# Optimization experiments

Measured on AMD Instinct MI355X. Metric: run time of the kernel, lower is better.

Reference implementation:

```python
import jax, jax.numpy as jnp
import numpy as np

B, N, L, K = 2, 16384, 256, 4
DIN, DOUT, DLAT, H, A, NH = 2, 3, 64, 128, 32, 4
PI = float(np.pi)

def _lin(key, din, dout, std=None):
    k1, k2 = jax.random.split(key)
    if std is None:
        lim = 1.0 / np.sqrt(din)
        w = jax.random.uniform(k1, (din, dout), minval=-lim, maxval=lim)
        b = jax.random.uniform(k2, (dout,), minval=-lim, maxval=lim)
        return w, b
    return jax.random.normal(k1, (din, dout)) * std

def setup_inputs() -> dict:
    key = jax.random.key(0)
    ks = jax.random.split(key, 16)
    x = jax.random.uniform(ks[0], (B, N, DIN)) * 2.0 - 1.0
    p = jax.random.uniform(ks[1], (B, L, DIN)) * 2.0 - 1.0
    c = jax.random.normal(ks[2], (B, L, DLAT))
    g = jax.random.uniform(ks[3], (B, L, 1)) * 0.5 + 0.1
    W_stem, b_stem = _lin(ks[4], DLAT, H)
    Wq_sin = _lin(ks[5], DIN, H // 2, std=2.0)
    Wq1, bq1 = _lin(ks[6], H + DIN, H)
    Wq2, bq2 = _lin(ks[7], H, NH * A)
    Wv_sin = _lin(ks[8], DIN, H // 2, std=20.0)
    Wv1, bv1 = _lin(ks[9], H + DIN, H)
    Wv2, bv2 = _lin(ks[10], H, 2 * H)
    Wk, bk = _lin(ks[11], H, NH * A)
    Wv, bv = _lin(ks[12], H, NH * H)
    Wo1, bo1 = _lin(ks[13], NH * H, NH * H)
    Wo2, bo2 = _lin(ks[14], NH * H, DOUT)
    return dict(x=x, p=p, c=c, g=g, W_stem=W_stem, b_stem=b_stem,
                Wq_sin=Wq_sin, Wq1=Wq1, bq1=bq1, Wq2=Wq2, bq2=bq2,
                Wv_sin=Wv_sin, Wv1=Wv1, bv1=bv1, Wv2=Wv2, bv2=bv2,
                Wk=Wk, bk=bk, Wv=Wv, bv=bv, Wo1=Wo1, bo1=bo1, Wo2=Wo2, bo2=bo2)

def _sin_emb(coords, W):
    c = PI * (coords + 1.0)
    e = c @ W
    return jnp.sin(jnp.concatenate([c, e, e + PI / 2.0], axis=-1))

def _emb_mlp(coords, Wsin, W1, b1, W2, b2):
    h = _sin_emb(coords, Wsin)
    h = jax.nn.gelu(h @ W1 + b1, approximate=False)
    return h @ W2 + b2

def _gather(t, idx):
    # t: [B,L,D], idx: [B,N,K] -> [B,N,K,D]
    return jax.vmap(lambda tb, ib: tb[ib])(t, idx)

def reference(x, p, c, g, W_stem, b_stem, Wq_sin, Wq1, bq1, Wq2, bq2,
              Wv_sin, Wv1, bv1, Wv2, bv2, Wk, bk, Wv, bv, Wo1, bo1, Wo2, bo2):
    c = c @ W_stem + b_stem                       # [B,L,H]
    k = c @ Wk + bk                               # [B,L,NH*A]
    rel_pos = x[:, :, None, :] - p[:, None, :, :] # [B,N,L,2]
    zx = jnp.sum(rel_pos ** 2, axis=-1)           # [B,N,L]
    idx = jnp.argsort(zx, axis=-1)[:, :, :K]      # [B,N,K]
    zx_k = jnp.take_along_axis(zx, idx, axis=2)[..., None]            # [B,N,K,1]
    rel_k = jnp.take_along_axis(rel_pos, idx[..., None], axis=2)      # [B,N,K,2]
    c_k = _gather(c, idx)                         # [B,N,K,H]
    k_k = _gather(k, idx)                         # [B,N,K,NH*A]
    g_k = _gather(g, idx)                         # [B,N,K,1]
    q = _emb_mlp(rel_k, Wq_sin, Wq1, bq1, Wq2, bq2)                   # [B,N,K,NH*A]
    vgb = _emb_mlp(rel_k, Wv_sin, Wv1, bv1, Wv2, bv2)                 # [B,N,K,2H]
    v_g, v_b = vgb[..., :H], vgb[..., H:]
    v = (c_k * v_g + v_b) @ Wv + bv               # [B,N,K,NH*H]
    q = q.reshape(B, N, K, NH, A)
    k_k = k_k.reshape(B, N, K, NH, A)
    v = v.reshape(B, N, K, NH, H)
    logits = jnp.sum(q * k_k, axis=-1, keepdims=True) \
             - ((1.0 / g_k ** 2) * zx_k)[..., None, :]                # [B,N,K,NH,1]
    att = jax.nn.softmax(logits, axis=2)
    y = jnp.sum(att * v, axis=2).reshape(B, N, NH * H)
    y = jax.nn.gelu(y @ Wo1 + bo1, approximate=False)
    return y @ Wo2 + bo2                          # [B,N,3]
```

## Files before the change

kernel.cpp:

```cpp
#include <hip/hip_runtime.h>
#include <math.h>

typedef unsigned short U16;
typedef unsigned int u32;
typedef unsigned long long u64;
typedef __attribute__((ext_vector_type(8))) short short8;
typedef __attribute__((ext_vector_type(4))) float f4;

#define LPTS   256
#define MFMA16(a,b,c) __builtin_amdgcn_mfma_f32_16x16x32_bf16(a, b, c, 0, 0, 0)

__device__ __forceinline__ float bf2f(U16 u) {
  return __uint_as_float(((unsigned int)u) << 16);
}
__device__ __forceinline__ U16 f2bf(float f) {
  unsigned int x = __float_as_uint(f);
  return (U16)((x + 0x7fffu + ((x >> 16) & 1u)) >> 16);
}
__device__ __forceinline__ float gelu_f(float v) {
  float z = fabsf(v) * 0.70710678f;
  float t = __builtin_amdgcn_rcpf(fmaf(0.3275911f, z, 1.0f));
  float poly = t * fmaf(t, fmaf(t, fmaf(t, fmaf(t, 1.061405429f, -1.453152027f),
                                        1.421413741f), -0.284496736f), 0.254829592f);
  float e = __expf(-z * z);
  float erf_abs = fmaf(-poly, e, 1.0f);
  float erf_s = copysignf(erf_abs, v);
  return 0.5f * v * (1.0f + erf_s);
}
__device__ __forceinline__ void ins4(u32& k0, u32& k1, u32& k2, u32& k3, u32 key) {
  if (key < k3) {
    if (key < k0)      { k3 = k2; k2 = k1; k1 = k0; k0 = key; }
    else if (key < k1) { k3 = k2; k2 = k1; k1 = key; }
    else if (key < k2) { k3 = k2; k2 = key; }
    else               { k3 = key; }
  }
}
__device__ __forceinline__ float ldf(const void* s, int i, int mode) {
  return mode ? bf2f(((const U16*)s)[i]) : ((const float*)s)[i];
}
__device__ __forceinline__ int wave_sniff(const void* w4) {
  int lane = threadIdx.x & 63;
  float v = bf2f(((const U16*)w4)[2 * lane]);
  u64 m = __ballot(fabsf(v) <= 0.1251f);
  return (__popcll(m) >= 56) ? 1 : 0;
}

struct PackArgs {
  const void* src[6];
  int K[6], N[6], KS[6];
  int base[7];
};

__global__ __launch_bounds__(256) void enf_prep(PackArgs pa,
    const void* c, const void* Wst, const void* bst, const void* Wkp, const void* bkp,
    float* __restrict__ cp_ws, float* __restrict__ kk_ws, U16* __restrict__ P)
{
  __shared__ float c_s[2][64];
  __shared__ float cp_s[2][128];
  const int t = threadIdx.x;
  const int mode = wave_sniff(Wst);
  const int bid = blockIdx.x;
  if (bid < 204) {
    int u = bid * 256 + t;
    if (u < pa.base[6]) {
      int s = 0;
      while (u >= pa.base[s + 1]) ++s;
      int rel = u - pa.base[s];
      int lane8 = rel & 63, rest = rel >> 6;
      int ks = rest % pa.KS[s], nt = rest / pa.KS[s];
      int kb = ks * 32 + ((lane8 >> 4) * 8);
      int n  = nt * 16 + (lane8 & 15);
      U16 vv[8];
#pragma unroll
      for (int j = 0; j < 8; ++j) {
        int k = kb + j;
        U16 v = 0;
        if (k < pa.K[s]) {
          int off = k * pa.N[s] + n;
          v = mode ? ((const U16*)pa.src[s])[off] : f2bf(((const float*)pa.src[s])[off]);
        }
        vv[j] = v;
      }
      *(short8*)(P + (size_t)u * 8) = *(short8*)vv;
    }
  } else {
    const int half = t >> 7, tl = t & 127;
    const int row = (bid - 204) * 2 + half;
    if (tl < 64) c_s[half][tl] = ldf(c, row * 64 + tl, mode);
    __syncthreads();
    float acc = 0.f;
#pragma unroll 8
    for (int i = 0; i < 64; ++i) acc = fmaf(c_s[half][i], ldf(Wst, i * 128 + tl, mode), acc);
    float cpv = acc + ldf(bst, tl, mode);
    cp_s[half][tl] = cpv;
    cp_ws[row * 128 + tl] = cpv;
    __syncthreads();
    acc = 0.f;
#pragma unroll 8
    for (int i = 0; i < 128; ++i) acc = fmaf(cp_s[half][i], ldf(Wkp, i * 128 + tl, mode), acc);
    kk_ws[row * 128 + tl] = acc + ldf(bkp, tl, mode);
  }
}

__global__ __launch_bounds__(512, 4) void enf_main(
    const void* __restrict__ w4,
    const void* __restrict__ x, const void* __restrict__ p, const void* __restrict__ g,
    const void* __restrict__ Wq_sin, const void* __restrict__ Wv_sin,
    const U16* __restrict__ PWq1, const void* __restrict__ bq1,
    const U16* __restrict__ PWq2, const void* __restrict__ bq2,
    const U16* __restrict__ PWv1, const void* __restrict__ bv1,
    const U16* __restrict__ PWv2, const void* __restrict__ bv2,
    const U16* __restrict__ PWv, const void* __restrict__ bv,
    const U16* __restrict__ PWo1, const void* __restrict__ bo1,
    const void* __restrict__ Wo2, const void* __restrict__ bo2,
    const float* __restrict__ cp_ws, const float* __restrict__ kk_ws,
    void* __restrict__ outp)
{
  __shared__ __align__(16) U16 poolS[128 * 168];
  __shared__ __align__(16) U16 poolH[128 * 132];
  __shared__ float wsin_s[128];
  __shared__ float xq[64];
  __shared__ float selDx[128], selDy[128], selB[128];
  __shared__ float att_s[128 * 4];
  __shared__ U16   selL[128];
  const int t = threadIdx.x;
  const int w = t >> 6, lane = t & 63;
  const int quad = lane >> 4, cl = lane & 15;
  const int qbase = blockIdx.x * 32;
  const int b = qbase >> 14;
  const int mode = wave_sniff(w4);
  float* p_sh = (float*)poolS;

  if (t < 64) xq[t] = ldf(x, qbase * 2 + t, mode);
  if (t < 128) wsin_s[t] = ldf(Wq_sin, t, mode);
  p_sh[t] = ldf(p, b * LPTS * 2 + t, mode);
  __syncthreads();

  {
    const int q = t >> 4;
    const float x0 = xq[q * 2 + 0], x1 = xq[q * 2 + 1];
    const int j = t & 15;
    u32 k0 = ~0u, k1 = ~0u, k2 = ~0u, k3 = ~0u;
#pragma unroll
    for (int s = 0; s < 16; ++s) {
      const int l = j * 16 + s;
      float dx = __fsub_rn(x0, p_sh[l * 2 + 0]);
      float dy = __fsub_rn(x1, p_sh[l * 2 + 1]);
      float d  = __fadd_rn(__fmul_rn(dx, dx), __fmul_rn(dy, dy));
      u32 key = (__float_as_uint(d) & 0xFFFFFF00u) | (u32)l;
      ins4(k0, k1, k2, k3, key);
    }
#pragma unroll
    for (int d = 1; d <= 8; d <<= 1) {
      u32 p0 = __shfl_xor(k0, d, 16);
      u32 p1 = __shfl_xor(k1, d, 16);
      u32 p2 = __shfl_xor(k2, d, 16);
      u32 p3 = __shfl_xor(k3, d, 16);
      ins4(k0, k1, k2, k3, p0); ins4(k0, k1, k2, k3, p1);
      ins4(k0, k1, k2, k3, p2); ins4(k0, k1, k2, k3, p3);
    }
    if (j == 0) {
      u32 sel[4] = { k0, k1, k2, k3 };
#pragma unroll
      for (int k = 0; k < 4; ++k) {
        int l = (int)(sel[k] & 255u);
        int r = q * 4 + k;
        selL[r]  = (U16)l;
        float dx = __fsub_rn(x0, p_sh[l * 2 + 0]);
        float dy = __fsub_rn(x1, p_sh[l * 2 + 1]);
        float zx = __fadd_rn(__fmul_rn(dx, dx), __fmul_rn(dy, dy));
        selDx[r] = dx;
        selDy[r] = dy;
        float gf = ldf(g, b * LPTS + l, mode);
        selB[r]  = __fmul_rn(1.0f / __fmul_rn(gf, gf), zx);
      }
    }
  }
  __syncthreads();

  {
    const int r = t >> 2, ln = t & 3;
    const float dx = selDx[r], dy = selDy[r];
    const float c0 = 3.14159274f * (dx + 1.0f);
    const float c1 = 3.14159274f * (dy + 1.0f);
    if (ln == 0) poolS[r * 168 + 0] = f2bf(__sinf(c0));
    if (ln == 1) poolS[r * 168 + 1] = f2bf(__sinf(c1));
#pragma unroll 1
    for (int i = ln; i < 64; i += 4) {
      float e = __fadd_rn(__fmul_rn(c0, wsin_s[i]), __fmul_rn(c1, wsin_s[64 + i]));
      poolS[r * 168 + 2 + i]  = f2bf(__sinf(e));
      poolS[r * 168 + 66 + i] = f2bf(__sinf(e + 1.57079637f));
    }
#pragma unroll 1
    for (int i = 130 + ln; i < 160; i += 4) poolS[r * 168 + i] = 0;
  }
  __syncthreads();

  if (t < 128) wsin_s[t] = ldf(Wv_sin, t, mode);
  {
    f4 acc[8];
#pragma unroll
    for (int i = 0; i < 8; ++i) acc[i] = (f4){0.f, 0.f, 0.f, 0.f};
    const U16* pb0 = PWq1 + ((w * 5) * 64 + lane) * 8;
    short8 b0 = *(const short8*)(pb0);
#pragma unroll 1
    for (int ks = 0; ks < 5; ++ks) {
      short8 n0 = *(const short8*)(pb0 + (ks + 1) * 512);
#pragma unroll
      for (int mt = 0; mt < 8; ++mt) {
        short8 a = *(const short8*)(poolS + (mt * 16 + cl) * 168 + quad * 8 + ks * 32);
        acc[mt] = MFMA16(a, b0, acc[mt]);
      }
      b0 = n0;
    }
    int col = w * 16 + cl;
    float bb = ldf(bq1, col, mode);
#pragma unroll
    for (int mt = 0; mt < 8; ++mt)
#pragma unroll
      for (int reg = 0; reg < 4; ++reg)
        poolH[(mt * 16 + quad * 4 + reg) * 132 + col] = f2bf(gelu_f(acc[mt][reg] + bb));
  }
  __syncthreads();

  if (w < 4) {
    const int wl = w;
    f4 acc[2][8];
#pragma unroll
    for (int i = 0; i < 8; ++i) { acc[0][i] = (f4){0.f,0.f,0.f,0.f}; acc[1][i] = (f4){0.f,0.f,0.f,0.f}; }
    const U16* pb0 = PWq2 + ((2 * wl + 0) * 4 * 64 + lane) * 8;
    const U16* pb1 = PWq2 + ((2 * wl + 1) * 4 * 64 + lane) * 8;
    short8 b0 = *(const short8*)(pb0);
    short8 b1 = *(const short8*)(pb1);
#pragma unroll 1
    for (int ks = 0; ks < 4; ++ks) {
      short8 n0 = *(const short8*)(pb0 + (ks + 1) * 512);
      short8 n1 = *(const short8*)(pb1 + (ks + 1) * 512);
#pragma unroll
      for (int mt = 0; mt < 8; ++mt) {
        short8 a = *(const short8*)(poolH + (mt * 16 + cl) * 132 + quad * 8 + ks * 32);
        acc[0][mt] = MFMA16(a, b0, acc[0][mt]);
        acc[1][mt] = MFMA16(a, b1, acc[1][mt]);
      }
      b0 = n0; b1 = n1;
    }
    const float bq2c0 = ldf(bq2, (2 * wl + 0) * 16 + cl, mode);
    const float bq2c1 = ldf(bq2, (2 * wl + 1) * 16 + cl, mode);
    const float* kkb = kk_ws + (size_t)b * LPTS * 128;
#pragma unroll
    for (int mt = 0; mt < 8; ++mt) {
      float part[4];
#pragma unroll
      for (int reg = 0; reg < 4; ++reg) {
        int r = mt * 16 + quad * 4 + reg;
        const float* kr = kkb + selL[r] * 128;
        float q0 = acc[0][mt][reg] + bq2c0;
        float q1 = acc[1][mt][reg] + bq2c1;
        part[reg] = __fmul_rn(q0, kr[(2 * wl + 0) * 16 + cl]);
        part[reg] = fmaf(q1, kr[(2 * wl + 1) * 16 + cl], part[reg]);
      }
#pragma unroll
      for (int d = 1; d <= 8; d <<= 1) {
        part[0] += __shfl_xor(part[0], d, 16);
        part[1] += __shfl_xor(part[1], d, 16);
        part[2] += __shfl_xor(part[2], d, 16);
        part[3] += __shfl_xor(part[3], d, 16);
      }
      if (cl == 0) {
        int q = mt * 4 + quad;
        float lg[4];
#pragma unroll
        for (int reg = 0; reg < 4; ++reg)
          lg[reg] = part[reg] - selB[q * 4 + reg];
        float m = fmaxf(fmaxf(lg[0], lg[1]), fmaxf(lg[2], lg[3]));
        float e0 = __expf(lg[0] - m), e1 = __expf(lg[1] - m);
        float e2 = __expf(lg[2] - m), e3 = __expf(lg[3] - m);
        float s = ((e0 + e1) + e2) + e3;
        att_s[(q * 4 + 0) * 4 + wl] = e0 / s;
        att_s[(q * 4 + 1) * 4 + wl] = e1 / s;
        att_s[(q * 4 + 2) * 4 + wl] = e2 / s;
        att_s[(q * 4 + 3) * 4 + wl] = e3 / s;
      }
    }
  } else {
    const int tt = t - 256;
    const int r = tt >> 1, ln = tt & 1;
    const float dx = selDx[r], dy = selDy[r];
    const float c0 = 3.14159274f * (dx + 1.0f);
    const float c1 = 3.14159274f * (dy + 1.0f);
    if (ln == 0) poolS[r * 168 + 0] = f2bf(__sinf(c0));
    if (ln == 1) poolS[r * 168 + 1] = f2bf(__sinf(c1));
#pragma unroll 1
    for (int i = ln; i < 64; i += 2) {
      float e = __fadd_rn(__fmul_rn(c0, wsin_s[i]), __fmul_rn(c1, wsin_s[64 + i]));
      poolS[r * 168 + 2 + i]  = f2bf(__sinf(e));
      poolS[r * 168 + 66 + i] = f2bf(__sinf(e + 1.57079637f));
    }
#pragma unroll 1
    for (int i = 130 + ln; i < 160; i += 2) poolS[r * 168 + i] = 0;
  }
  __syncthreads();

  {
    f4 acc[8];
#pragma unroll
    for (int i = 0; i < 8; ++i) acc[i] = (f4){0.f, 0.f, 0.f, 0.f};
    const U16* pb0 = PWv1 + ((w * 5) * 64 + lane) * 8;
    short8 b0 = *(const short8*)(pb0);
#pragma unroll 1
    for (int ks = 0; ks < 5; ++ks) {
      short8 n0 = *(const short8*)(pb0 + (ks + 1) * 512);
#pragma unroll
      for (int mt = 0; mt < 8; ++mt) {
        short8 a = *(const short8*)(poolS + (mt * 16 + cl) * 168 + quad * 8 + ks * 32);
        acc[mt] = MFMA16(a, b0, acc[mt]);
      }
      b0 = n0;
    }
    int col = w * 16 + cl;
    float bb = ldf(bv1, col, mode);
#pragma unroll
    for (int mt = 0; mt < 8; ++mt)
#pragma unroll
      for (int reg = 0; reg < 4; ++reg)
        poolH[(mt * 16 + quad * 4 + reg) * 132 + col] = f2bf(gelu_f(acc[mt][reg] + bb));
  }
  __syncthreads();

  {
    f4 ag[8], ab[8];
#pragma unroll
    for (int i = 0; i < 8; ++i) { ag[i] = (f4){0.f,0.f,0.f,0.f}; ab[i] = (f4){0.f,0.f,0.f,0.f}; }
    const U16* pg = PWv2 + ((w * 4) * 64 + lane) * 8;
    const U16* pb = PWv2 + (((8 + w) * 4) * 64 + lane) * 8;
    short8 bg = *(const short8*)(pg);
    short8 bb2 = *(const short8*)(pb);
#pragma unroll 1
    for (int ks = 0; ks < 4; ++ks) {
      short8 ng = *(const short8*)(pg + (ks + 1) * 512);
      short8 nb = *(const short8*)(pb + (ks + 1) * 512);
#pragma unroll
      for (int mt = 0; mt < 8; ++mt) {
        short8 a = *(const short8*)(poolH + (mt * 16 + cl) * 132 + quad * 8 + ks * 32);
        ag[mt] = MFMA16(a, bg, ag[mt]);
        ab[mt] = MFMA16(a, bb2, ab[mt]);
      }
      bg = ng; bb2 = nb;
    }
    int col = w * 16 + cl;
    float bgb = ldf(bv2, col, mode), bbb = ldf(bv2, 128 + col, mode);
#pragma unroll
    for (int mt = 0; mt < 8; ++mt)
#pragma unroll
      for (int reg = 0; reg < 4; ++reg) {
        int row = mt * 16 + quad * 4 + reg;
        float cp = cp_ws[(b * LPTS + selL[row]) * 128 + col];
        float vin = __fadd_rn(__fmul_rn(cp, ag[mt][reg] + bgb), ab[mt][reg] + bbb);
        poolS[row * 132 + col] = f2bf(vin);
      }
  }
  __syncthreads();

  {
    const int gqh = t >> 2, sl = t & 3;
    const int q = gqh & 31, h = gqh >> 5;
    float a0 = att_s[(q * 4 + 0) * 4 + h];
    float a1 = att_s[(q * 4 + 1) * 4 + h];
    float a2 = att_s[(q * 4 + 2) * 4 + h];
    float a3 = att_s[(q * 4 + 3) * 4 + h];
#pragma unroll 1
    for (int j = 0; j < 8; ++j) {
      int e0 = j * 16 + sl * 4;
      ushort4 v0 = *(const ushort4*)(poolS + (q * 4 + 0) * 132 + e0);
      ushort4 v1 = *(const ushort4*)(poolS + (q * 4 + 1) * 132 + e0);
      ushort4 v2 = *(const ushort4*)(poolS + (q * 4 + 2) * 132 + e0);
      ushort4 v3 = *(const ushort4*)(poolS + (q * 4 + 3) * 132 + e0);
      ushort4 o;
      o.x = f2bf(fmaf(a3, bf2f(v3.x), fmaf(a2, bf2f(v2.x), fmaf(a1, bf2f(v1.x), a0 * bf2f(v0.x)))));
      o.y = f2bf(fmaf(a3, bf2f(v3.y), fmaf(a2, bf2f(v2.y), fmaf(a1, bf2f(v1.y), a0 * bf2f(v0.y)))));
      o.z = f2bf(fmaf(a3, bf2f(v3.z), fmaf(a2, bf2f(v2.z), fmaf(a1, bf2f(v1.z), a0 * bf2f(v0.z)))));
      o.w = f2bf(fmaf(a3, bf2f(v3.w), fmaf(a2, bf2f(v2.w), fmaf(a1, bf2f(v1.w), a0 * bf2f(v0.w)))));
      *(ushort4*)(poolH + (h * 32 + q) * 132 + e0) = o;
    }
  }
  __syncthreads();

  U16* ySt = poolS;
  {
    f4 acc5[2][4];
#pragma unroll
    for (int i = 0; i < 4; ++i) { acc5[0][i] = (f4){0.f,0.f,0.f,0.f}; acc5[1][i] = (f4){0.f,0.f,0.f,0.f}; }
    const int h = w >> 1;
    const int nt0 = h * 8 + (w & 1) * 4;
    const U16* a5p = poolH + (h * 32 + cl) * 132 + quad * 8;
    short8 cb[4], nb[4];
#pragma unroll
    for (int ntl = 0; ntl < 4; ++ntl)
      cb[ntl] = *(const short8*)(PWv + ((nt0 + ntl) * 4 * 64 + lane) * 8);
#pragma unroll 1
    for (int ks = 0; ks < 4; ++ks) {
#pragma unroll
      for (int ntl = 0; ntl < 4; ++ntl)
        nb[ntl] = *(const short8*)(PWv + (((nt0 + ntl) * 4 + ks + 1) * 64 + lane) * 8);
#pragma unroll
      for (int mt = 0; mt < 2; ++mt) {
        short8 a = *(const short8*)(a5p + mt * 16 * 132 + ks * 32);
#pragma unroll
        for (int ntl = 0; ntl < 4; ++ntl) acc5[mt][ntl] = MFMA16(a, cb[ntl], acc5[mt][ntl]);
      }
#pragma unroll
      for (int ntl = 0; ntl < 4; ++ntl) cb[ntl] = nb[ntl];
    }
#pragma unroll
    for (int ntl = 0; ntl < 4; ++ntl) {
      int col = (nt0 + ntl) * 16 + cl;
      float bbv = ldf(bv, col, mode);
#pragma unroll
      for (int mt = 0; mt < 2; ++mt)
#pragma unroll
        for (int reg = 0; reg < 4; ++reg) {
          int q = mt * 16 + quad * 4 + reg;
          ySt[q * 520 + col] = f2bf(acc5[mt][ntl][reg] + bbv);
        }
    }
  }
  __syncthreads();

  {
    f4 acc[2][4];
#pragma unroll
    for (int i = 0; i < 4; ++i) { acc[0][i] = (f4){0.f,0.f,0.f,0.f}; acc[1][i] = (f4){0.f,0.f,0.f,0.f}; }
    const U16* aP = ySt + cl * 520 + quad * 8;
    const U16* bP = PWo1 + ((w * 4) * 16 * 64 + lane) * 8;
    short8 cb[4], nb[4];
#pragma unroll
    for (int ntl = 0; ntl < 4; ++ntl)
      cb[ntl] = *(const short8*)(bP + (ntl * 16) * 512);
#pragma unroll 1
    for (int ks = 0; ks < 16; ++ks) {
#pragma unroll
      for (int ntl = 0; ntl < 4; ++ntl)
        nb[ntl] = *(const short8*)(bP + (ntl * 16 + ks + 1) * 512);
#pragma unroll
      for (int mt = 0; mt < 2; ++mt) {
        short8 a = *(const short8*)(aP + mt * 16 * 520 + ks * 32);
#pragma unroll
        for (int ntl = 0; ntl < 4; ++ntl) acc[mt][ntl] = MFMA16(a, cb[ntl], acc[mt][ntl]);
      }
#pragma unroll
      for (int ntl = 0; ntl < 4; ++ntl) cb[ntl] = nb[ntl];
    }
    float oacc[2][4][3];
#pragma unroll
    for (int mt = 0; mt < 2; ++mt)
#pragma unroll
      for (int reg = 0; reg < 4; ++reg) { oacc[mt][reg][0]=0.f; oacc[mt][reg][1]=0.f; oacc[mt][reg][2]=0.f; }
#pragma unroll
    for (int ntl = 0; ntl < 4; ++ntl) {
      int col = (w * 4 + ntl) * 16 + cl;
      float bb = ldf(bo1, col, mode);
      float w0 = ldf(Wo2, col * 3 + 0, mode);
      float w1 = ldf(Wo2, col * 3 + 1, mode);
      float w2 = ldf(Wo2, col * 3 + 2, mode);
#pragma unroll
      for (int mt = 0; mt < 2; ++mt)
#pragma unroll
        for (int reg = 0; reg < 4; ++reg) {
          float y2 = gelu_f(acc[mt][ntl][reg] + bb);
          oacc[mt][reg][0] = fmaf(y2, w0, oacc[mt][reg][0]);
          oacc[mt][reg][1] = fmaf(y2, w1, oacc[mt][reg][1]);
          oacc[mt][reg][2] = fmaf(y2, w2, oacc[mt][reg][2]);
        }
    }
    float* obuf = (float*)poolH;
#pragma unroll
    for (int mt = 0; mt < 2; ++mt)
#pragma unroll
      for (int reg = 0; reg < 4; ++reg)
#pragma unroll
        for (int cix = 0; cix < 3; ++cix) {
          float v = oacc[mt][reg][cix];
          v += __shfl_xor(v, 1);
          v += __shfl_xor(v, 2);
          v += __shfl_xor(v, 4);
          v += __shfl_xor(v, 8);
          if (cl == 0) obuf[(w * 32 + mt * 16 + quad * 4 + reg) * 3 + cix] = v;
        }
  }
  __syncthreads();
  if (t < 96) {
    float* obuf = (float*)poolH;
    int row = t / 3, cix = t - row * 3;
    float s = obuf[row * 3 + cix];
#pragma unroll
    for (int ww = 1; ww < 8; ++ww) s += obuf[(ww * 32 + row) * 3 + cix];
    float ov = s + ldf(bo2, cix, mode);
    int pos = (qbase + row) * 3 + cix;
    if (mode) ((U16*)outp)[pos] = f2bf(ov);
    else      ((float*)outp)[pos] = ov;
  }
}

extern "C" void kernel_launch(void* const* d_in, const int* in_sizes, int n_in,
                              void* d_out, int out_size, void* d_ws, size_t ws_size,
                              hipStream_t stream) {
  (void)in_sizes; (void)n_in; (void)out_size; (void)ws_size;

  float* ws     = (float*)d_ws;
  float* cp_ws  = ws;
  float* kk_ws  = ws + 65536;
  U16*   Pbase  = (U16*)(ws + 131072);
  U16*   PWq1   = Pbase + 0;
  U16*   PWq2   = Pbase + 20480;
  U16*   PWv1   = Pbase + 36864;
  U16*   PWv2   = Pbase + 57344;
  U16*   PWv    = Pbase + 90112;
  U16*   PWo1   = Pbase + 155648;

  PackArgs pa;
  const int psrc[6] = {7, 9, 12, 14, 18, 20};
  static const int pK[6]  = {130, 128, 130, 128, 128, 512};
  static const int pN[6]  = {128, 128, 128, 256, 512, 512};
  static const int pKS[6] = {5, 4, 5, 4, 4, 16};
  static const int pB8[7] = {0, 2560, 4608, 7168, 11264, 19456, 52224};
  for (int i = 0; i < 6; ++i) {
    pa.src[i] = d_in[psrc[i]];
    pa.K[i] = pK[i]; pa.N[i] = pN[i]; pa.KS[i] = pKS[i]; pa.base[i] = pB8[i];
  }
  pa.base[6] = pB8[6];

  hipLaunchKernelGGL(enf_prep, dim3(460), dim3(256), 0, stream,
                     pa, d_in[2], d_in[4], d_in[5], d_in[16], d_in[17],
                     cp_ws, kk_ws, Pbase);
  hipLaunchKernelGGL(enf_main, dim3(1024), dim3(512), 0, stream,
                     d_in[4],
                     d_in[0], d_in[1], d_in[3],
                     d_in[6], d_in[11],
                     PWq1, d_in[8],  PWq2, d_in[10],
                     PWv1, d_in[13], PWv2, d_in[15],
                     PWv,  d_in[19],
                     PWo1, d_in[21], d_in[22], d_in[23],
                     cp_ws, kk_ws, (void*)d_out);
}
```

Measured before the change: 268.4 us.

## Prefetch first weight fragments before barriers and pack bf16 stores

Issues the first global load of each stage's MFMA weight fragment before the preceding __syncthreads, so its latency overlaps the barrier wait. Sinusoidal embedding and attention-weighted sum writes now use v_cvt_pk_bf16_f32 packed 32-bit LDS stores instead of scalar 16-bit stores, and the distance loop reads p as float2. This adds register pressure from the live prefetched fragments. The packed conversion may round differently from the manual f2bf.

```diff
diff --git a/kernel.cpp b/kernel.cpp
--- a/kernel.cpp
+++ b/kernel.cpp
@@ -16,6 +16,11 @@
 __device__ __forceinline__ U16 f2bf(float f) {
   unsigned int x = __float_as_uint(f);
   return (U16)((x + 0x7fffu + ((x >> 16) & 1u)) >> 16);
+}
+__device__ __forceinline__ u32 pk_bf16(float lo, float hi) {
+  u32 r;
+  asm("v_cvt_pk_bf16_f32 %0, %1, %2" : "=v"(r) : "v"(lo), "v"(hi));
+  return r;
 }
 __device__ __forceinline__ float gelu_f(float v) {
   float z = fabsf(v) * 0.70710678f;
@@ -144,8 +149,9 @@
 #pragma unroll
     for (int s = 0; s < 16; ++s) {
       const int l = j * 16 + s;
-      float dx = __fsub_rn(x0, p_sh[l * 2 + 0]);
-      float dy = __fsub_rn(x1, p_sh[l * 2 + 1]);
+      float2 pp = *(const float2*)&p_sh[l * 2];
+      float dx = __fsub_rn(x0, pp.x);
+      float dy = __fsub_rn(x1, pp.y);
       float d  = __fadd_rn(__fmul_rn(dx, dx), __fmul_rn(dy, dy));
       u32 key = (__float_as_uint(d) & 0xFFFFFF00u) | (u32)l;
       ins4(k0, k1, k2, k3, key);
@@ -183,26 +189,30 @@
     const float dx = selDx[r], dy = selDy[r];
     const float c0 = 3.14159274f * (dx + 1.0f);
     const float c1 = 3.14159274f * (dy + 1.0f);
-    if (ln == 0) poolS[r * 168 + 0] = f2bf(__sinf(c0));
-    if (ln == 1) poolS[r * 168 + 1] = f2bf(__sinf(c1));
-#pragma unroll 1
-    for (int i = ln; i < 64; i += 4) {
-      float e = __fadd_rn(__fmul_rn(c0, wsin_s[i]), __fmul_rn(c1, wsin_s[64 + i]));
-      poolS[r * 168 + 2 + i]  = f2bf(__sinf(e));
-      poolS[r * 168 + 66 + i] = f2bf(__sinf(e + 1.57079637f));
-    }
-#pragma unroll 1
-    for (int i = 130 + ln; i < 160; i += 4) poolS[r * 168 + i] = 0;
-  }
-  __syncthreads();
-
-  if (t < 128) wsin_s[t] = ldf(Wv_sin, t, mode);
+    U16* rowp = poolS + r * 168;
+    if (ln == 0) rowp[0] = f2bf(__sinf(c0));
+    if (ln == 1) rowp[1] = f2bf(__sinf(c1));
+#pragma unroll 1
+    for (int i = ln * 16; i < ln * 16 + 16; i += 2) {
+      float e0 = __fadd_rn(__fmul_rn(c0, wsin_s[i]),     __fmul_rn(c1, wsin_s[64 + i]));
+      float e1 = __fadd_rn(__fmul_rn(c0, wsin_s[i + 1]), __fmul_rn(c1, wsin_s[64 + i + 1]));
+      *(u32*)(rowp + 2 + i)  = pk_bf16(__sinf(e0), __sinf(e1));
+      *(u32*)(rowp + 66 + i) = pk_bf16(__sinf(e0 + 1.57079637f), __sinf(e1 + 1.57079637f));
+    }
+#pragma unroll 1
+    for (int k = ln; k < 15; k += 4) *(u32*)(rowp + 130 + 2 * k) = 0;
+  }
+  float wv_tmp = (t < 128) ? ldf(Wv_sin, t, mode) : 0.f;
+  short8 h4b0 = *(const short8*)(PWq1 + ((w * 5) * 64 + lane) * 8);
+  __syncthreads();
+
+  if (t < 128) wsin_s[t] = wv_tmp;
   {
     f4 acc[8];
 #pragma unroll
     for (int i = 0; i < 8; ++i) acc[i] = (f4){0.f, 0.f, 0.f, 0.f};
     const U16* pb0 = PWq1 + ((w * 5) * 64 + lane) * 8;
-    short8 b0 = *(const short8*)(pb0);
+    short8 b0 = h4b0;
 #pragma unroll 1
     for (int ks = 0; ks < 5; ++ks) {
       short8 n0 = *(const short8*)(pb0 + (ks + 1) * 512);
@@ -221,6 +231,8 @@
       for (int reg = 0; reg < 4; ++reg)
         poolH[(mt * 16 + quad * 4 + reg) * 132 + col] = f2bf(gelu_f(acc[mt][reg] + bb));
   }
+  short8 h5b0 = *(const short8*)(PWq2 + ((2 * (w & 3) + 0) * 4 * 64 + lane) * 8);
+  short8 h5b1 = *(const short8*)(PWq2 + ((2 * (w & 3) + 1) * 4 * 64 + lane) * 8);
   __syncthreads();
 
   if (w < 4) {
@@ -230,8 +242,8 @@
     for (int i = 0; i < 8; ++i) { acc[0][i] = (f4){0.f,0.f,0.f,0.f}; acc[1][i] = (f4){0.f,0.f,0.f,0.f}; }
     const U16* pb0 = PWq2 + ((2 * wl + 0) * 4 * 64 + lane) * 8;
     const U16* pb1 = PWq2 + ((2 * wl + 1) * 4 * 64 + lane) * 8;
-    short8 b0 = *(const short8*)(pb0);
-    short8 b1 = *(const short8*)(pb1);
+    short8 b0 = h5b0;
+    short8 b1 = h5b1;
 #pragma unroll 1
     for (int ks = 0; ks < 4; ++ks) {
       short8 n0 = *(const short8*)(pb0 + (ks + 1) * 512);
@@ -284,21 +296,24 @@
     }
   } else {
     const int tt = t - 256;
-    const int r = tt >> 1, ln = tt & 1;
+    const int r = tt >> 1, ln2 = tt & 1;
     const float dx = selDx[r], dy = selDy[r];
     const float c0 = 3.14159274f * (dx + 1.0f);
     const float c1 = 3.14159274f * (dy + 1.0f);
-    if (ln == 0) poolS[r * 168 + 0] = f2bf(__sinf(c0));
-    if (ln == 1) poolS[r * 168 + 1] = f2bf(__sinf(c1));
-#pragma unroll 1
-    for (int i = ln; i < 64; i += 2) {
-      float e = __fadd_rn(__fmul_rn(c0, wsin_s[i]), __fmul_rn(c1, wsin_s[64 + i]));
-      poolS[r * 168 + 2 + i]  = f2bf(__sinf(e));
-      poolS[r * 168 + 66 + i] = f2bf(__sinf(e + 1.57079637f));
-    }
-#pragma unroll 1
-    for (int i = 130 + ln; i < 160; i += 2) poolS[r * 168 + i] = 0;
-  }
+    U16* rowp = poolS + r * 168;
+    if (ln2 == 0) rowp[0] = f2bf(__sinf(c0));
+    if (ln2 == 1) rowp[1] = f2bf(__sinf(c1));
+#pragma unroll 1
+    for (int i = ln2 * 32; i < ln2 * 32 + 32; i += 2) {
+      float e0 = __fadd_rn(__fmul_rn(c0, wsin_s[i]),     __fmul_rn(c1, wsin_s[64 + i]));
+      float e1 = __fadd_rn(__fmul_rn(c0, wsin_s[i + 1]), __fmul_rn(c1, wsin_s[64 + i + 1]));
+      *(u32*)(rowp + 2 + i)  = pk_bf16(__sinf(e0), __sinf(e1));
+      *(u32*)(rowp + 66 + i) = pk_bf16(__sinf(e0 + 1.57079637f), __sinf(e1 + 1.57079637f));
+    }
+#pragma unroll 1
+    for (int k = ln2; k < 15; k += 2) *(u32*)(rowp + 130 + 2 * k) = 0;
+  }
+  short8 h6b0 = *(const short8*)(PWv1 + ((w * 5) * 64 + lane) * 8);
   __syncthreads();
 
   {
@@ -306,7 +321,7 @@
 #pragma unroll
     for (int i = 0; i < 8; ++i) acc[i] = (f4){0.f, 0.f, 0.f, 0.f};
     const U16* pb0 = PWv1 + ((w * 5) * 64 + lane) * 8;
-    short8 b0 = *(const short8*)(pb0);
+    short8 b0 = h6b0;
 #pragma unroll 1
     for (int ks = 0; ks < 5; ++ks) {
       short8 n0 = *(const short8*)(pb0 + (ks + 1) * 512);
@@ -325,6 +340,8 @@
       for (int reg = 0; reg < 4; ++reg)
         poolH[(mt * 16 + quad * 4 + reg) * 132 + col] = f2bf(gelu_f(acc[mt][reg] + bb));
   }
+  short8 h7g = *(const short8*)(PWv2 + ((w * 4) * 64 + lane) * 8);
+  short8 h7b = *(const short8*)(PWv2 + (((8 + w) * 4) * 64 + lane) * 8);
   __syncthreads();
 
   {
@@ -333,8 +350,8 @@
     for (int i = 0; i < 8; ++i) { ag[i] = (f4){0.f,0.f,0.f,0.f}; ab[i] = (f4){0.f,0.f,0.f,0.f}; }
     const U16* pg = PWv2 + ((w * 4) * 64 + lane) * 8;
     const U16* pb = PWv2 + (((8 + w) * 4) * 64 + lane) * 8;
-    short8 bg = *(const short8*)(pg);
-    short8 bb2 = *(const short8*)(pb);
+    short8 bg = h7g;
+    short8 bb2 = h7b;
 #pragma unroll 1
     for (int ks = 0; ks < 4; ++ks) {
       short8 ng = *(const short8*)(pg + (ks + 1) * 512);
@@ -359,6 +376,10 @@
         poolS[row * 132 + col] = f2bf(vin);
       }
   }
+  short8 h9cb0 = *(const short8*)(PWv + (((w >> 1) * 8 + (w & 1) * 4 + 0) * 4 * 64 + lane) * 8);
+  short8 h9cb1 = *(const short8*)(PWv + (((w >> 1) * 8 + (w & 1) * 4 + 1) * 4 * 64 + lane) * 8);
+  short8 h9cb2 = *(const short8*)(PWv + (((w >> 1) * 8 + (w & 1) * 4 + 2) * 4 * 64 + lane) * 8);
+  short8 h9cb3 = *(const short8*)(PWv + (((w >> 1) * 8 + (w & 1) * 4 + 3) * 4 * 64 + lane) * 8);
   __syncthreads();
 
   {
@@ -375,12 +396,14 @@
       ushort4 v1 = *(const ushort4*)(poolS + (q * 4 + 1) * 132 + e0);
       ushort4 v2 = *(const ushort4*)(poolS + (q * 4 + 2) * 132 + e0);
       ushort4 v3 = *(const ushort4*)(poolS + (q * 4 + 3) * 132 + e0);
-      ushort4 o;
-      o.x = f2bf(fmaf(a3, bf2f(v3.x), fmaf(a2, bf2f(v2.x), fmaf(a1, bf2f(v1.x), a0 * bf2f(v0.x)))));
-      o.y = f2bf(fmaf(a3, bf2f(v3.y), fmaf(a2, bf2f(v2.y), fmaf(a1, bf2f(v1.y), a0 * bf2f(v0.y)))));
-      o.z = f2bf(fmaf(a3, bf2f(v3.z), fmaf(a2, bf2f(v2.z), fmaf(a1, bf2f(v1.z), a0 * bf2f(v0.z)))));
-      o.w = f2bf(fmaf(a3, bf2f(v3.w), fmaf(a2, bf2f(v2.w), fmaf(a1, bf2f(v1.w), a0 * bf2f(v0.w)))));
-      *(ushort4*)(poolH + (h * 32 + q) * 132 + e0) = o;
+      float s0 = fmaf(a3, bf2f(v3.x), fmaf(a2, bf2f(v2.x), fmaf(a1, bf2f(v1.x), a0 * bf2f(v0.x))));
+      float s1 = fmaf(a3, bf2f(v3.y), fmaf(a2, bf2f(v2.y), fmaf(a1, bf2f(v1.y), a0 * bf2f(v0.y))));
+      float s2 = fmaf(a3, bf2f(v3.z), fmaf(a2, bf2f(v2.z), fmaf(a1, bf2f(v1.z), a0 * bf2f(v0.z))));
+      float s3 = fmaf(a3, bf2f(v3.w), fmaf(a2, bf2f(v2.w), fmaf(a1, bf2f(v1.w), a0 * bf2f(v0.w))));
+      uint2 o;
+      o.x = pk_bf16(s0, s1);
+      o.y = pk_bf16(s2, s3);
+      *(uint2*)(poolH + (h * 32 + q) * 132 + e0) = o;
     }
   }
   __syncthreads();
@@ -394,9 +417,7 @@
     const int nt0 = h * 8 + (w & 1) * 4;
     const U16* a5p = poolH + (h * 32 + cl) * 132 + quad * 8;
     short8 cb[4], nb[4];
-#pragma unroll
-    for (int ntl = 0; ntl < 4; ++ntl)
-      cb[ntl] = *(const short8*)(PWv + ((nt0 + ntl) * 4 * 64 + lane) * 8);
+    cb[0] = h9cb0; cb[1] = h9cb1; cb[2] = h9cb2; cb[3] = h9cb3;
 #pragma unroll 1
     for (int ks = 0; ks < 4; ++ks) {
 #pragma unroll
@@ -424,6 +445,10 @@
         }
     }
   }
+  short8 hAcb0 = *(const short8*)(PWo1 + (((w * 4 + 0) * 16) * 64 + lane) * 8);
+  short8 hAcb1 = *(const short8*)(PWo1 + (((w * 4 + 1) * 16) * 64 + lane) * 8);
+  short8 hAcb2 = *(const short8*)(PWo1 + (((w * 4 + 2) * 16) * 64 + lane) * 8);
+  short8 hAcb3 = *(const short8*)(PWo1 + (((w * 4 + 3) * 16) * 64 + lane) * 8);
   __syncthreads();
 
   {
@@ -433,9 +458,7 @@
     const U16* aP = ySt + cl * 520 + quad * 8;
     const U16* bP = PWo1 + ((w * 4) * 16 * 64 + lane) * 8;
     short8 cb[4], nb[4];
-#pragma unroll
-    for (int ntl = 0; ntl < 4; ++ntl)
-      cb[ntl] = *(const short8*)(bP + (ntl * 16) * 512);
+    cb[0] = hAcb0; cb[1] = hAcb1; cb[2] = hAcb2; cb[3] = hAcb3;
 #pragma unroll 1
     for (int ks = 0; ks < 16; ++ks) {
 #pragma unroll
```

Result: no change. 268.0 us (-0.1%).
